# Kernel tuning notes

Hardware: AMD Instinct MI355X
Metric: run time of the kernel (lower is better)

The kernel has to match this reference:

```python
import jax, jax.numpy as jnp
import numpy as np

COMMITMENT_COST = 0.25


def setup_inputs() -> dict:
    key = jax.random.key(0)
    k1, k2 = jax.random.split(key)
    z_e = jax.random.normal(k1, (32, 256, 32, 32), dtype=jnp.float32)
    codebook = jax.random.normal(k2, (1024, 256), dtype=jnp.float32)
    return {"z_e": z_e, "codebook": codebook}


def reference(z_e, codebook):
    B, D, H, W = z_e.shape
    # (B, D, H, W) -> (N, D), N = B*H*W
    z_flat = jnp.transpose(z_e, (0, 2, 3, 1)).reshape(-1, D)
    # squared L2 distances to every codebook entry: (N, K)
    distances = (
        jnp.sum(z_flat * z_flat, axis=1, keepdims=True)
        - 2.0 * (z_flat @ codebook.T)
        + jnp.sum(codebook * codebook, axis=1)
    )
    codes = jnp.argmin(distances, axis=1)          # (N,)
    z_q = jnp.transpose(codebook[codes].reshape(B, H, W, D), (0, 3, 1, 2))
    # straight-through estimator
    z_q_st = z_e + jax.lax.stop_gradient(z_q - z_e)
    codebook_loss = jnp.mean((jax.lax.stop_gradient(z_q) - z_e) ** 2)
    commitment_loss = jnp.mean((z_q - jax.lax.stop_gradient(z_e)) ** 2)
    vq_loss = codebook_loss + COMMITMENT_COST * commitment_loss
    indices = codes.reshape(B, H, W)
    return z_q_st, indices, vq_loss
```

## Files before the change

### kernel.cpp

```cpp
#include <hip/hip_runtime.h>
#include <cstdint>
#include <cstddef>


typedef __attribute__((ext_vector_type(8))) short bf16x8;
typedef __attribute__((ext_vector_type(4))) float f32x4;

#define GL2LDS(g, l) __builtin_amdgcn_global_load_lds( \
    (__attribute__((address_space(1))) const void*)(g), \
    (__attribute__((address_space(3))) void*)(l), 16, 0, 0)

__device__ __forceinline__ unsigned short rne_bf16(float f) {
    unsigned u = __float_as_uint(f);
    return (unsigned short)((u + 0x7FFFu + ((u >> 16) & 1u)) >> 16);
}
__device__ __forceinline__ float bf16_to_f(unsigned short h) {
    return __uint_as_float((unsigned)h << 16);
}

__global__ __launch_bounds__(256)
void vq_cnorm_kernel(const float* __restrict__ cb, float* __restrict__ cnorm)
{
    const int k = blockIdx.x * 256 + threadIdx.x;
    const float4* row = reinterpret_cast<const float4*>(cb + (size_t)k * 256);
    float s0 = 0.f, s1 = 0.f, s2 = 0.f, s3 = 0.f;
#pragma unroll 8
    for (int i = 0; i < 64; ++i) {
        float4 v = row[i];
        s0 = fmaf(v.x, v.x, s0);
        s1 = fmaf(v.y, v.y, s1);
        s2 = fmaf(v.z, v.z, s2);
        s3 = fmaf(v.w, v.w, s3);
    }
    cnorm[k] = (s0 + s1) + (s2 + s3);
}

__global__ __launch_bounds__(256)
void vq_csplit_kernel(const float* __restrict__ cb, unsigned short* __restrict__ c0,
                      unsigned short* __restrict__ c1, unsigned short* __restrict__ c2,
                      unsigned long long* __restrict__ packed, float* __restrict__ loss)
{
    const int b = blockIdx.x, t = threadIdx.x;
    const int idx = b * 256 + t;
    if (t < 128) packed[b * 128 + t] = 0xFFFFFFFFFFFFFFFFull;
    if (b == 0 && t == 255) *loss = 0.f;

    float4 v = reinterpret_cast<const float4*>(cb)[idx];
    float f[4] = { v.x, v.y, v.z, v.w };
    ushort4 h0, h1, h2;
    unsigned short* p0[4] = { &h0.x, &h0.y, &h0.z, &h0.w };
    unsigned short* p1[4] = { &h1.x, &h1.y, &h1.z, &h1.w };
    unsigned short* p2[4] = { &h2.x, &h2.y, &h2.z, &h2.w };
#pragma unroll
    for (int j = 0; j < 4; ++j) {
        unsigned short b0 = rne_bf16(f[j]); float r1 = f[j] - bf16_to_f(b0);
        unsigned short b1 = rne_bf16(r1);   float r2 = r1 - bf16_to_f(b1);
        unsigned short b2 = rne_bf16(r2);
        *p0[j] = b0; *p1[j] = b1; *p2[j] = b2;
    }
    reinterpret_cast<ushort4*>(c0)[idx] = h0;
    reinterpret_cast<ushort4*>(c1)[idx] = h1;
    reinterpret_cast<ushort4*>(c2)[idx] = h2;
}

__global__ __launch_bounds__(256)
void vq_zsplit_kernel(const float* __restrict__ z, unsigned short* __restrict__ z0,
                      unsigned short* __restrict__ z1, unsigned short* __restrict__ z2)
{
    __shared__ float zl[64 * 264];
    const int t = threadIdx.x, blk = blockIdx.x;
    const int b = blk >> 4, hw0 = (blk & 15) << 6;
    const float* zb = z + ((size_t)b << 18) + hw0;
#pragma unroll 8
    for (int i = 0; i < 64; ++i) {
        int idx = i * 256 + t;
        int d = idx >> 6, hwl = idx & 63;
        zl[hwl * 264 + d] = zb[(size_t)d * 1024 + hwl];
    }
    __syncthreads();
    const int n0 = (b << 10) + hw0;
#pragma unroll
    for (int p = 0; p < 8; ++p) {
        const int hwl = p * 8 + (t >> 5);
        const int d0 = (t & 31) * 8;
        const float* src = &zl[hwl * 264 + d0];
        unsigned short h0[8], h1[8], h2[8];
#pragma unroll
        for (int j = 0; j < 8; ++j) {
            float f = src[j];
            unsigned short b0 = rne_bf16(f);  float r1 = f - bf16_to_f(b0);
            unsigned short b1 = rne_bf16(r1); float r2 = r1 - bf16_to_f(b1);
            unsigned short b2 = rne_bf16(r2);
            h0[j] = b0; h1[j] = b1; h2[j] = b2;
        }
        const size_t o = (size_t)(n0 + hwl) * 256 + d0;
        ushort4 a;
        a = ushort4{h0[0],h0[1],h0[2],h0[3]}; *reinterpret_cast<ushort4*>(z0 + o)     = a;
        a = ushort4{h0[4],h0[5],h0[6],h0[7]}; *reinterpret_cast<ushort4*>(z0 + o + 4) = a;
        a = ushort4{h1[0],h1[1],h1[2],h1[3]}; *reinterpret_cast<ushort4*>(z1 + o)     = a;
        a = ushort4{h1[4],h1[5],h1[6],h1[7]}; *reinterpret_cast<ushort4*>(z1 + o + 4) = a;
        a = ushort4{h2[0],h2[1],h2[2],h2[3]}; *reinterpret_cast<ushort4*>(z2 + o)     = a;
        a = ushort4{h2[4],h2[5],h2[6],h2[7]}; *reinterpret_cast<ushort4*>(z2 + o + 4) = a;
    }
}

__global__ __launch_bounds__(512, 2)
void vq_mfma_argmin_kernel(const unsigned short* __restrict__ zp,
                           const unsigned short* __restrict__ cp,
                           const float* __restrict__ cnorm,
                           unsigned long long* __restrict__ packed)
{
    __shared__ unsigned short Ld[2][2][2][256 * 32];

    const int tid = threadIdx.x, l = tid & 63, w = tid >> 6;
    const int wr = w >> 2, wc = w & 3;
    const int nid = ((blockIdx.x & 7) << 6) | (blockIdx.x >> 3);
    const int bm = nid >> 2, bn = nid & 3;
    const int arow = bm * 256, brow = bn * 256;

    f32x4 acc[8][4];
#pragma unroll
    for (int m = 0; m < 8; ++m)
#pragma unroll
        for (int n = 0; n < 4; ++n) acc[m][n] = f32x4{0.f, 0.f, 0.f, 0.f};

    const int srow  = l >> 2;
    const int selem = (((l & 3) ^ ((l >> 3) & 3))) << 3;

    const int lo16 = l & 15, hi4 = l >> 4;
    const int fco = ((hi4 ^ ((lo16 >> 1) & 3))) << 3;

#define STAGE(tt, mat, kk) do {                                               \
    const int seg_ = (tt) >> 2;                                               \
    const unsigned short* S_ = (mat)                                          \
        ? cp + (size_t)((0x211000 >> (seg_ << 2)) & 3) * 262144u              \
        : zp + (size_t)((0x010210 >> (seg_ << 2)) & 3) * 8388608u;            \
    const int R_  = (mat) ? brow : arow;                                      \
    const int KO_ = (((tt) & 3) << 6) + ((kk) << 5) + selem;                  \
    GL2LDS(S_ + (size_t)(R_ + (w * 2 + 0) * 16 + srow) * 256 + KO_,           \
           &Ld[(tt) & 1][mat][kk][(w * 2 + 0) * 512]);                        \
    GL2LDS(S_ + (size_t)(R_ + (w * 2 + 1) * 16 + srow) * 256 + KO_,           \
           &Ld[(tt) & 1][mat][kk][(w * 2 + 1) * 512]);                        \
} while (0)

#define VM4  asm volatile("s_waitcnt vmcnt(4)"  ::: "memory")
#define VM0  asm volatile("s_waitcnt vmcnt(0)"  ::: "memory")
#define NOPS ((void)0)
#define FNCE do { asm volatile("" ::: "memory");                              \
                  __builtin_amdgcn_sched_barrier(0); } while (0)
#define SBAR do { asm volatile("" ::: "memory");                              \
                  __builtin_amdgcn_s_barrier();                               \
                  __builtin_amdgcn_sched_barrier(0); } while (0)

#define PH(t, mh, kk, STAGESTMT, VMSTMT, BARSTMT) do {                        \
    const unsigned short* Ap_ = &Ld[(t) & 1][0][kk][0];                       \
    const unsigned short* Bp_ = &Ld[(t) & 1][1][kk][0];                       \
    bf16x8 a0, a1, a2, a3, b0, b1, b2, b3;                                    \
    a0 = *(const bf16x8*)&Ap_[(wr*128 + ((mh)*4+0)*16 + lo16)*32 + fco];      \
    a1 = *(const bf16x8*)&Ap_[(wr*128 + ((mh)*4+1)*16 + lo16)*32 + fco];      \
    a2 = *(const bf16x8*)&Ap_[(wr*128 + ((mh)*4+2)*16 + lo16)*32 + fco];      \
    a3 = *(const bf16x8*)&Ap_[(wr*128 + ((mh)*4+3)*16 + lo16)*32 + fco];      \
    b0 = *(const bf16x8*)&Bp_[(wc*64 + 0*16 + lo16)*32 + fco];                \
    b1 = *(const bf16x8*)&Bp_[(wc*64 + 1*16 + lo16)*32 + fco];                \
    b2 = *(const bf16x8*)&Bp_[(wc*64 + 2*16 + lo16)*32 + fco];                \
    b3 = *(const bf16x8*)&Bp_[(wc*64 + 3*16 + lo16)*32 + fco];                \
    STAGESTMT;                                                                \
    FNCE;                                                                     \
    __builtin_amdgcn_s_setprio(1);                                            \
    acc[(mh)*4+0][0] = __builtin_amdgcn_mfma_f32_16x16x32_bf16(a0, b0, acc[(mh)*4+0][0], 0,0,0); \
    acc[(mh)*4+0][1] = __builtin_amdgcn_mfma_f32_16x16x32_bf16(a0, b1, acc[(mh)*4+0][1], 0,0,0); \
    acc[(mh)*4+0][2] = __builtin_amdgcn_mfma_f32_16x16x32_bf16(a0, b2, acc[(mh)*4+0][2], 0,0,0); \
    acc[(mh)*4+0][3] = __builtin_amdgcn_mfma_f32_16x16x32_bf16(a0, b3, acc[(mh)*4+0][3], 0,0,0); \
    acc[(mh)*4+1][0] = __builtin_amdgcn_mfma_f32_16x16x32_bf16(a1, b0, acc[(mh)*4+1][0], 0,0,0); \
    acc[(mh)*4+1][1] = __builtin_amdgcn_mfma_f32_16x16x32_bf16(a1, b1, acc[(mh)*4+1][1], 0,0,0); \
    acc[(mh)*4+1][2] = __builtin_amdgcn_mfma_f32_16x16x32_bf16(a1, b2, acc[(mh)*4+1][2], 0,0,0); \
    acc[(mh)*4+1][3] = __builtin_amdgcn_mfma_f32_16x16x32_bf16(a1, b3, acc[(mh)*4+1][3], 0,0,0); \
    acc[(mh)*4+2][0] = __builtin_amdgcn_mfma_f32_16x16x32_bf16(a2, b0, acc[(mh)*4+2][0], 0,0,0); \
    acc[(mh)*4+2][1] = __builtin_amdgcn_mfma_f32_16x16x32_bf16(a2, b1, acc[(mh)*4+2][1], 0,0,0); \
    acc[(mh)*4+2][2] = __builtin_amdgcn_mfma_f32_16x16x32_bf16(a2, b2, acc[(mh)*4+2][2], 0,0,0); \
    acc[(mh)*4+2][3] = __builtin_amdgcn_mfma_f32_16x16x32_bf16(a2, b3, acc[(mh)*4+2][3], 0,0,0); \
    acc[(mh)*4+3][0] = __builtin_amdgcn_mfma_f32_16x16x32_bf16(a3, b0, acc[(mh)*4+3][0], 0,0,0); \
    acc[(mh)*4+3][1] = __builtin_amdgcn_mfma_f32_16x16x32_bf16(a3, b1, acc[(mh)*4+3][1], 0,0,0); \
    acc[(mh)*4+3][2] = __builtin_amdgcn_mfma_f32_16x16x32_bf16(a3, b2, acc[(mh)*4+3][2], 0,0,0); \
    acc[(mh)*4+3][3] = __builtin_amdgcn_mfma_f32_16x16x32_bf16(a3, b3, acc[(mh)*4+3][3], 0,0,0); \
    __builtin_amdgcn_s_setprio(0);                                            \
    VMSTMT;                                                                   \
    BARSTMT;                                                                  \
} while (0)

#define TILE(t, SA0, SB0, SA1, SB1, V2, V4)                                   \
    PH(t, 0, 0, SA0, NOPS, FNCE);                                             \
    PH(t, 1, 0, SB0, V2,   SBAR);                                             \
    PH(t, 0, 1, SA1, NOPS, FNCE);                                             \
    PH(t, 1, 1, SB1, V4,   SBAR)

    STAGE(0, 0, 0); STAGE(0, 1, 0); STAGE(0, 0, 1); STAGE(0, 1, 1);
    VM4;
    SBAR;

#pragma unroll 2
    for (int t = 0; t <= 22; ++t) {
        TILE(t, STAGE(t + 1, 0, 0), STAGE(t + 1, 1, 0),
                STAGE(t + 1, 0, 1), STAGE(t + 1, 1, 1), VM4, VM4);
    }
    TILE(23, NOPS, NOPS, NOPS, NOPS, VM0, NOPS);

#undef TILE
#undef PH
#undef STAGE

    int coln[4]; float cnv[4];
#pragma unroll
    for (int n = 0; n < 4; ++n) {
        coln[n] = brow + wc * 64 + n * 16 + lo16;
        cnv[n] = cnorm[coln[n]];
    }
#pragma unroll
    for (int m = 0; m < 8; ++m) {
#pragma unroll
        for (int j = 0; j < 4; ++j) {
            unsigned long long best = 0xFFFFFFFFFFFFFFFFull;
#pragma unroll
            for (int n = 0; n < 4; ++n) {
                float d = fmaf(-2.0f, acc[m][n][j], cnv[n]);
                unsigned u = __float_as_uint(d);
                u = (u & 0x80000000u) ? ~u : (u | 0x80000000u);
                unsigned long long pk = ((unsigned long long)u << 32) | (unsigned)coln[n];
                best = pk < best ? pk : best;
            }
#pragma unroll
            for (int mask = 1; mask <= 8; mask <<= 1) {
                unsigned long long o = __shfl_xor(best, mask, 64);
                best = o < best ? o : best;
            }
            if (lo16 == 0) {
                const int row = arow + wr * 128 + m * 16 + hi4 * 4 + j;
                atomicMin(&packed[row], best);
            }
        }
    }
}

__global__ __launch_bounds__(256, 2)
void vq_gather_packed_kernel(const float* __restrict__ cb, const float* __restrict__ z,
                             const unsigned long long* __restrict__ packed,
                             float* __restrict__ out_zq, float* __restrict__ out_idx,
                             float* __restrict__ loss)
{
    __shared__ float rows[64 * 257];
    __shared__ int   ks[64];
    __shared__ float wsum[4];

    const int t   = threadIdx.x;
    const int blk = blockIdx.x;
    const int b   = blk >> 4;
    const int hw0 = (blk & 15) << 6;
    const int n0  = blk << 6;

    if (t < 64) {
        const int k = (int)(packed[n0 + t] & 0xFFFFFFFFull);
        ks[t] = k;
        out_idx[n0 + t] = (float)k;
    }
    __syncthreads();

#pragma unroll 4
    for (int i = 0; i < 64; ++i) {
        rows[i * 257 + t] = cb[(size_t)ks[i] * 256 + t];
    }
    __syncthreads();

    const int dq = t >> 6;
    const int hw = t & 63;
    const size_t obase = ((size_t)b << 18) + hw0 + hw;
    float sum = 0.f;
#pragma unroll 4
    for (int dd = 0; dd < 64; ++dd) {
        const int d = (dq << 6) + dd;
        const float  q  = rows[hw * 257 + d];
        const size_t a  = obase + (size_t)d * 1024;
        const float  zv = z[a];
        out_zq[a] = q;
        const float diff = q - zv;
        sum = fmaf(diff, diff, sum);
    }
#pragma unroll
    for (int m = 1; m <= 32; m <<= 1) sum += __shfl_xor(sum, m, 64);
    if ((t & 63) == 0) wsum[t >> 6] = sum;
    __syncthreads();
    if (t == 0) {
        const float s = (wsum[0] + wsum[1]) + (wsum[2] + wsum[3]);
        atomicAdd(loss, s * (1.25f / 8388608.0f));
    }
}

__global__ __launch_bounds__(256)
void vq_transpose_kernel(const float* __restrict__ cb, float* __restrict__ ctT)
{
    __shared__ float tile[64 * 65];
    const int t  = threadIdx.x;
    const int kb = blockIdx.x >> 2, db = blockIdx.x & 3;
    const int k0 = kb << 6, d0 = db << 6;
#pragma unroll
    for (int i = 0; i < 16; ++i) {
        int idx = i * 256 + t;
        int r = idx >> 6, c = idx & 63;
        tile[r * 65 + c] = cb[(size_t)(k0 + r) * 256 + d0 + c];
    }
    __syncthreads();
#pragma unroll
    for (int i = 0; i < 16; ++i) {
        int idx = i * 256 + t;
        int r = idx >> 6, c = idx & 63;
        ctT[(size_t)(d0 + r) * 1024 + k0 + c] = tile[c * 65 + r];
    }
}

__global__ __launch_bounds__(256)
void vq_cnorm_fb_kernel(const float* __restrict__ cb, float* __restrict__ cnorm)
{
    const int k = blockIdx.x * 256 + threadIdx.x;
    const float4* row = reinterpret_cast<const float4*>(cb + (size_t)k * 256);
    float s0 = 0.f, s1 = 0.f, s2 = 0.f, s3 = 0.f;
#pragma unroll 8
    for (int i = 0; i < 64; ++i) {
        float4 v = row[i];
        s0 = fmaf(v.x, v.x, s0);
        s1 = fmaf(v.y, v.y, s1);
        s2 = fmaf(v.z, v.z, s2);
        s3 = fmaf(v.w, v.w, s3);
    }
    cnorm[k] = (s0 + s1) + (s2 + s3);
}

__global__ __launch_bounds__(512, 2)
void vq_argmin_kernel(const float* __restrict__ z, const float* __restrict__ ctT,
                      const float* __restrict__ cnorm, int* __restrict__ codes,
                      float* __restrict__ out_idx)
{
    __shared__ float zt[256 * 64];
    __shared__ float ct[16 * 256];
    const int t = threadIdx.x, tx = t & 63, ty = t >> 6, p0 = ty << 3;
    const int blk = blockIdx.x, b = blk >> 4, hw0 = (blk & 15) << 6;
    const float* zbase = z + ((size_t)b << 18) + hw0;
#pragma unroll
    for (int i = 0; i < 8; ++i) {
        int idx = i * 512 + t;
        int d = idx >> 4, c4 = (idx & 15) << 2;
        float4 v = *reinterpret_cast<const float4*>(zbase + (size_t)d * 1024 + c4);
        *reinterpret_cast<float4*>(&zt[d * 64 + c4]) = v;
    }
    float minv[8]; int mini[8];
#pragma unroll
    for (int i = 0; i < 8; ++i) { minv[i] = 3.0e38f; mini[i] = 0; }
    const float* zrd = &zt[p0];
    const float* crd = &ct[tx << 2];
    for (int kt = 0; kt < 4; ++kt) {
        const int k0 = kt << 8;
        float acc[8][4];
#pragma unroll
        for (int i = 0; i < 8; ++i)
#pragma unroll
            for (int j = 0; j < 4; ++j) acc[i][j] = 0.f;
        for (int dc = 0; dc < 16; ++dc) {
            const int d0 = dc << 4;
            __syncthreads();
#pragma unroll
            for (int i = 0; i < 2; ++i) {
                int idx = i * 512 + t;
                int r = idx >> 6, c4 = (idx & 63) << 2;
                float4 v = *reinterpret_cast<const float4*>(ctT + (size_t)(d0 + r) * 1024 + k0 + c4);
                *reinterpret_cast<float4*>(&ct[r * 256 + c4]) = v;
            }
            __syncthreads();
            const float* zp = zrd + d0 * 64;
#pragma unroll
            for (int d = 0; d < 16; ++d) {
                float4 za = *reinterpret_cast<const float4*>(zp + d * 64);
                float4 zb = *reinterpret_cast<const float4*>(zp + d * 64 + 4);
                float4 cc = *reinterpret_cast<const float4*>(crd + d * 256);
#define VQ_FMA_ROW(ii, zv)                          \
                acc[ii][0] = fmaf(zv, cc.x, acc[ii][0]); \
                acc[ii][1] = fmaf(zv, cc.y, acc[ii][1]); \
                acc[ii][2] = fmaf(zv, cc.z, acc[ii][2]); \
                acc[ii][3] = fmaf(zv, cc.w, acc[ii][3]);
                VQ_FMA_ROW(0, za.x) VQ_FMA_ROW(1, za.y) VQ_FMA_ROW(2, za.z) VQ_FMA_ROW(3, za.w)
                VQ_FMA_ROW(4, zb.x) VQ_FMA_ROW(5, zb.y) VQ_FMA_ROW(6, zb.z) VQ_FMA_ROW(7, zb.w)
#undef VQ_FMA_ROW
            }
        }
#pragma unroll
        for (int j = 0; j < 4; ++j) {
            const int k = k0 + (tx << 2) + j;
            const float cn = cnorm[k];
#pragma unroll
            for (int i = 0; i < 8; ++i) {
                float dist = fmaf(-2.0f, acc[i][j], cn);
                if (dist < minv[i]) { minv[i] = dist; mini[i] = k; }
            }
        }
    }
#pragma unroll
    for (int m = 1; m <= 32; m <<= 1) {
#pragma unroll
        for (int i = 0; i < 8; ++i) {
            float ov = __shfl_xor(minv[i], m, 64);
            int   oi = __shfl_xor(mini[i], m, 64);
            if (ov < minv[i] || (ov == minv[i] && oi < mini[i])) { minv[i] = ov; mini[i] = oi; }
        }
    }
    if (tx == 0) {
        const int n0 = (blk << 6) + p0;
#pragma unroll
        for (int i = 0; i < 8; ++i) {
            codes[n0 + i]   = mini[i];
            out_idx[n0 + i] = (float)mini[i];
        }
    }
}

__global__ __launch_bounds__(256, 2)
void vq_gather_kernel(const float* __restrict__ cb, const float* __restrict__ z,
                      const int* __restrict__ codes, float* __restrict__ out_zq,
                      float* __restrict__ loss)
{
    __shared__ float rows[64 * 257];
    __shared__ int   ks[64];
    __shared__ float wsum[4];
    const int t = threadIdx.x, blk = blockIdx.x;
    const int b = blk >> 4, hw0 = (blk & 15) << 6, n0 = blk << 6;
    if (t < 64) ks[t] = codes[n0 + t];
    __syncthreads();
#pragma unroll 4
    for (int i = 0; i < 64; ++i) rows[i * 257 + t] = cb[(size_t)ks[i] * 256 + t];
    __syncthreads();
    const int dq = t >> 6, hw = t & 63;
    const size_t obase = ((size_t)b << 18) + hw0 + hw;
    float sum = 0.f;
#pragma unroll 4
    for (int dd = 0; dd < 64; ++dd) {
        const int d = (dq << 6) + dd;
        const float  q  = rows[hw * 257 + d];
        const size_t a  = obase + (size_t)d * 1024;
        const float  zv = z[a];
        out_zq[a] = q;
        const float diff = q - zv;
        sum = fmaf(diff, diff, sum);
    }
#pragma unroll
    for (int m = 1; m <= 32; m <<= 1) sum += __shfl_xor(sum, m, 64);
    if ((t & 63) == 0) wsum[t >> 6] = sum;
    __syncthreads();
    if (t == 0) {
        const float s = (wsum[0] + wsum[1]) + (wsum[2] + wsum[3]);
        atomicAdd(loss, s * (1.25f / 8388608.0f));
    }
}

extern "C" void kernel_launch(void* const* d_in, const int* in_sizes, int n_in,
                              void* d_out, int out_size, void* d_ws, size_t ws_size,
                              hipStream_t stream)
{
    (void)in_sizes; (void)n_in; (void)out_size;

    const float* z  = (const float*)d_in[0];
    const float* cb = (const float*)d_in[1];

    float* out      = (float*)d_out;
    float* out_zq   = out;
    float* out_idx  = out + 8388608;
    float* out_loss = out + 8421376;

    const size_t NEED = 262144ull + 3ull * 16777216ull + 3ull * 524288ull + 4096ull;

    if (ws_size >= NEED) {
        unsigned long long* packed = (unsigned long long*)d_ws;
        unsigned short* z0 = (unsigned short*)((char*)d_ws + 262144);
        unsigned short* z1 = z0 + 8388608u;
        unsigned short* z2 = z1 + 8388608u;
        unsigned short* c0 = z2 + 8388608u;
        unsigned short* c1 = c0 + 262144u;
        unsigned short* c2 = c1 + 262144u;
        float* cnorm = (float*)(c2 + 262144u);

        vq_csplit_kernel<<<256, 256, 0, stream>>>(cb, c0, c1, c2, packed, out_loss);
        vq_cnorm_kernel<<<4, 256, 0, stream>>>(cb, cnorm);
        vq_zsplit_kernel<<<512, 256, 0, stream>>>(z, z0, z1, z2);
        vq_mfma_argmin_kernel<<<512, 512, 0, stream>>>(z0, c0, cnorm, packed);
        vq_gather_packed_kernel<<<512, 256, 0, stream>>>(cb, z, packed, out_zq, out_idx, out_loss);
    } else {
        float* ctT   = (float*)d_ws;
        float* cnorm = ctT + 256 * 1024;
        int*   codes = (int*)(cnorm + 1024);

        hipMemsetAsync(out_loss, 0, sizeof(float), stream);
        vq_transpose_kernel<<<64, 256, 0, stream>>>(cb, ctT);
        vq_cnorm_fb_kernel<<<4, 256, 0, stream>>>(cb, cnorm);
        vq_argmin_kernel<<<512, 512, 0, stream>>>(z, ctT, cnorm, codes, out_idx);
        vq_gather_kernel<<<512, 256, 0, stream>>>(cb, z, codes, out_zq, out_loss);
    }
}
```

Measured before the change: 172.2 us.

## Retile argmin GEMM to 256x128 blocks with triple-buffered LDS pipeline

Shrinks each block's tile from 256x256 to 256x128 codes, doubling the grid to 1024 blocks and halving per-wave accumulators. Staging moves from a double buffer to a three-stage LDS ring, issuing six async global-to-LDS loads two tiles ahead with one barrier per K-step. The aim is deeper latency hiding and better load balance across CUs. In exchange the z operand is reloaded twice as often, the launch bound drops to one block per CU, and LDS per block grows to 144KB.

New measurement: 180.1 us. 4.6% more time.

```diff
diff --git a/kernel.cpp b/kernel.cpp
--- a/kernel.cpp
+++ b/kernel.cpp
@@ -104,23 +104,23 @@
     }
 }
 
-__global__ __launch_bounds__(512, 2)
+__global__ __launch_bounds__(512, 1)
 void vq_mfma_argmin_kernel(const unsigned short* __restrict__ zp,
                            const unsigned short* __restrict__ cp,
                            const float* __restrict__ cnorm,
                            unsigned long long* __restrict__ packed)
 {
-    __shared__ unsigned short Ld[2][2][2][256 * 32];
+    __shared__ unsigned short Ld[3 * 24576];
 
     const int tid = threadIdx.x, l = tid & 63, w = tid >> 6;
-    const int wr = w >> 2, wc = w & 3;
-    const int nid = ((blockIdx.x & 7) << 6) | (blockIdx.x >> 3);
-    const int bm = nid >> 2, bn = nid & 3;
-    const int arow = bm * 256, brow = bn * 256;
-
-    f32x4 acc[8][4];
-#pragma unroll
-    for (int m = 0; m < 8; ++m)
+    const int wr = w >> 1, wc = w & 1;
+    const int nid = ((blockIdx.x & 7) << 7) | (blockIdx.x >> 3);
+    const int bm = nid >> 3, bn = nid & 7;
+    const int arow = bm * 256, brow = bn * 128;
+
+    f32x4 acc[4][4];
+#pragma unroll
+    for (int m = 0; m < 4; ++m)
 #pragma unroll
         for (int n = 0; n < 4; ++n) acc[m][n] = f32x4{0.f, 0.f, 0.f, 0.f};
 
@@ -130,20 +130,20 @@
     const int lo16 = l & 15, hi4 = l >> 4;
     const int fco = ((hi4 ^ ((lo16 >> 1) & 3))) << 3;
 
-#define STAGE(tt, mat, kk) do {                                               \
+#define STAGE6(tt, BUFP) do {                                                 \
     const int seg_ = (tt) >> 2;                                               \
-    const unsigned short* S_ = (mat)                                          \
-        ? cp + (size_t)((0x211000 >> (seg_ << 2)) & 3) * 262144u              \
-        : zp + (size_t)((0x010210 >> (seg_ << 2)) & 3) * 8388608u;            \
-    const int R_  = (mat) ? brow : arow;                                      \
-    const int KO_ = (((tt) & 3) << 6) + ((kk) << 5) + selem;                  \
-    GL2LDS(S_ + (size_t)(R_ + (w * 2 + 0) * 16 + srow) * 256 + KO_,           \
-           &Ld[(tt) & 1][mat][kk][(w * 2 + 0) * 512]);                        \
-    GL2LDS(S_ + (size_t)(R_ + (w * 2 + 1) * 16 + srow) * 256 + KO_,           \
-           &Ld[(tt) & 1][mat][kk][(w * 2 + 1) * 512]);                        \
+    const unsigned short* As_ = zp + (size_t)((0x010210 >> (seg_ << 2)) & 3) * 8388608u; \
+    const unsigned short* Bs_ = cp + (size_t)((0x211000 >> (seg_ << 2)) & 3) * 262144u;  \
+    const int KO_ = (((tt) & 3) << 6) + selem;                                \
+    GL2LDS(As_ + (size_t)(arow + w * 32 +  0 + srow) * 256 + KO_,      (BUFP) + (w * 32     ) * 32); \
+    GL2LDS(As_ + (size_t)(arow + w * 32 + 16 + srow) * 256 + KO_,      (BUFP) + (w * 32 + 16) * 32); \
+    GL2LDS(As_ + (size_t)(arow + w * 32 +  0 + srow) * 256 + KO_ + 32, (BUFP) + 8192 + (w * 32     ) * 32); \
+    GL2LDS(As_ + (size_t)(arow + w * 32 + 16 + srow) * 256 + KO_ + 32, (BUFP) + 8192 + (w * 32 + 16) * 32); \
+    GL2LDS(Bs_ + (size_t)(brow + w * 16 + srow) * 256 + KO_,           (BUFP) + 16384 + (w * 16) * 32); \
+    GL2LDS(Bs_ + (size_t)(brow + w * 16 + srow) * 256 + KO_ + 32,      (BUFP) + 16384 + 4096 + (w * 16) * 32); \
 } while (0)
 
-#define VM4  asm volatile("s_waitcnt vmcnt(4)"  ::: "memory")
+#define VM6  asm volatile("s_waitcnt vmcnt(6)"  ::: "memory")
 #define VM0  asm volatile("s_waitcnt vmcnt(0)"  ::: "memory")
 #define NOPS ((void)0)
 #define FNCE do { asm volatile("" ::: "memory");                              \
@@ -152,14 +152,32 @@
                   __builtin_amdgcn_s_barrier();                               \
                   __builtin_amdgcn_sched_barrier(0); } while (0)
 
-#define PH(t, mh, kk, STAGESTMT, VMSTMT, BARSTMT) do {                        \
-    const unsigned short* Ap_ = &Ld[(t) & 1][0][kk][0];                       \
-    const unsigned short* Bp_ = &Ld[(t) & 1][1][kk][0];                       \
+#define MFMA16(A0, A1, A2, A3, B0, B1, B2, B3)                                \
+    acc[0][0] = __builtin_amdgcn_mfma_f32_16x16x32_bf16(A0, B0, acc[0][0], 0,0,0); \
+    acc[0][1] = __builtin_amdgcn_mfma_f32_16x16x32_bf16(A0, B1, acc[0][1], 0,0,0); \
+    acc[0][2] = __builtin_amdgcn_mfma_f32_16x16x32_bf16(A0, B2, acc[0][2], 0,0,0); \
+    acc[0][3] = __builtin_amdgcn_mfma_f32_16x16x32_bf16(A0, B3, acc[0][3], 0,0,0); \
+    acc[1][0] = __builtin_amdgcn_mfma_f32_16x16x32_bf16(A1, B0, acc[1][0], 0,0,0); \
+    acc[1][1] = __builtin_amdgcn_mfma_f32_16x16x32_bf16(A1, B1, acc[1][1], 0,0,0); \
+    acc[1][2] = __builtin_amdgcn_mfma_f32_16x16x32_bf16(A1, B2, acc[1][2], 0,0,0); \
+    acc[1][3] = __builtin_amdgcn_mfma_f32_16x16x32_bf16(A1, B3, acc[1][3], 0,0,0); \
+    acc[2][0] = __builtin_amdgcn_mfma_f32_16x16x32_bf16(A2, B0, acc[2][0], 0,0,0); \
+    acc[2][1] = __builtin_amdgcn_mfma_f32_16x16x32_bf16(A2, B1, acc[2][1], 0,0,0); \
+    acc[2][2] = __builtin_amdgcn_mfma_f32_16x16x32_bf16(A2, B2, acc[2][2], 0,0,0); \
+    acc[2][3] = __builtin_amdgcn_mfma_f32_16x16x32_bf16(A2, B3, acc[2][3], 0,0,0); \
+    acc[3][0] = __builtin_amdgcn_mfma_f32_16x16x32_bf16(A3, B0, acc[3][0], 0,0,0); \
+    acc[3][1] = __builtin_amdgcn_mfma_f32_16x16x32_bf16(A3, B1, acc[3][1], 0,0,0); \
+    acc[3][2] = __builtin_amdgcn_mfma_f32_16x16x32_bf16(A3, B2, acc[3][2], 0,0,0); \
+    acc[3][3] = __builtin_amdgcn_mfma_f32_16x16x32_bf16(A3, B3, acc[3][3], 0,0,0)
+
+#define PH_T(BUFP, STAGESTMT, VMSTMT, BARSTMT) do {                           \
+    const unsigned short* Ap_ = (BUFP);                                       \
+    const unsigned short* Bp_ = (BUFP) + 16384;                               \
     bf16x8 a0, a1, a2, a3, b0, b1, b2, b3;                                    \
-    a0 = *(const bf16x8*)&Ap_[(wr*128 + ((mh)*4+0)*16 + lo16)*32 + fco];      \
-    a1 = *(const bf16x8*)&Ap_[(wr*128 + ((mh)*4+1)*16 + lo16)*32 + fco];      \
-    a2 = *(const bf16x8*)&Ap_[(wr*128 + ((mh)*4+2)*16 + lo16)*32 + fco];      \
-    a3 = *(const bf16x8*)&Ap_[(wr*128 + ((mh)*4+3)*16 + lo16)*32 + fco];      \
+    a0 = *(const bf16x8*)&Ap_[(wr*64 + 0*16 + lo16)*32 + fco];                \
+    a1 = *(const bf16x8*)&Ap_[(wr*64 + 1*16 + lo16)*32 + fco];                \
+    a2 = *(const bf16x8*)&Ap_[(wr*64 + 2*16 + lo16)*32 + fco];                \
+    a3 = *(const bf16x8*)&Ap_[(wr*64 + 3*16 + lo16)*32 + fco];                \
     b0 = *(const bf16x8*)&Bp_[(wc*64 + 0*16 + lo16)*32 + fco];                \
     b1 = *(const bf16x8*)&Bp_[(wc*64 + 1*16 + lo16)*32 + fco];                \
     b2 = *(const bf16x8*)&Bp_[(wc*64 + 2*16 + lo16)*32 + fco];                \
@@ -167,47 +185,41 @@
     STAGESTMT;                                                                \
     FNCE;                                                                     \
     __builtin_amdgcn_s_setprio(1);                                            \
-    acc[(mh)*4+0][0] = __builtin_amdgcn_mfma_f32_16x16x32_bf16(a0, b0, acc[(mh)*4+0][0], 0,0,0); \
-    acc[(mh)*4+0][1] = __builtin_amdgcn_mfma_f32_16x16x32_bf16(a0, b1, acc[(mh)*4+0][1], 0,0,0); \
-    acc[(mh)*4+0][2] = __builtin_amdgcn_mfma_f32_16x16x32_bf16(a0, b2, acc[(mh)*4+0][2], 0,0,0); \
-    acc[(mh)*4+0][3] = __builtin_amdgcn_mfma_f32_16x16x32_bf16(a0, b3, acc[(mh)*4+0][3], 0,0,0); \
-    acc[(mh)*4+1][0] = __builtin_amdgcn_mfma_f32_16x16x32_bf16(a1, b0, acc[(mh)*4+1][0], 0,0,0); \
-    acc[(mh)*4+1][1] = __builtin_amdgcn_mfma_f32_16x16x32_bf16(a1, b1, acc[(mh)*4+1][1], 0,0,0); \
-    acc[(mh)*4+1][2] = __builtin_amdgcn_mfma_f32_16x16x32_bf16(a1, b2, acc[(mh)*4+1][2], 0,0,0); \
-    acc[(mh)*4+1][3] = __builtin_amdgcn_mfma_f32_16x16x32_bf16(a1, b3, acc[(mh)*4+1][3], 0,0,0); \
-    acc[(mh)*4+2][0] = __builtin_amdgcn_mfma_f32_16x16x32_bf16(a2, b0, acc[(mh)*4+2][0], 0,0,0); \
-    acc[(mh)*4+2][1] = __builtin_amdgcn_mfma_f32_16x16x32_bf16(a2, b1, acc[(mh)*4+2][1], 0,0,0); \
-    acc[(mh)*4+2][2] = __builtin_amdgcn_mfma_f32_16x16x32_bf16(a2, b2, acc[(mh)*4+2][2], 0,0,0); \
-    acc[(mh)*4+2][3] = __builtin_amdgcn_mfma_f32_16x16x32_bf16(a2, b3, acc[(mh)*4+2][3], 0,0,0); \
-    acc[(mh)*4+3][0] = __builtin_amdgcn_mfma_f32_16x16x32_bf16(a3, b0, acc[(mh)*4+3][0], 0,0,0); \
-    acc[(mh)*4+3][1] = __builtin_amdgcn_mfma_f32_16x16x32_bf16(a3, b1, acc[(mh)*4+3][1], 0,0,0); \
-    acc[(mh)*4+3][2] = __builtin_amdgcn_mfma_f32_16x16x32_bf16(a3, b2, acc[(mh)*4+3][2], 0,0,0); \
-    acc[(mh)*4+3][3] = __builtin_amdgcn_mfma_f32_16x16x32_bf16(a3, b3, acc[(mh)*4+3][3], 0,0,0); \
+    MFMA16(a0, a1, a2, a3, b0, b1, b2, b3);                                   \
+    __builtin_amdgcn_s_setprio(0);                                            \
+    a0 = *(const bf16x8*)&Ap_[8192 + (wr*64 + 0*16 + lo16)*32 + fco];         \
+    a1 = *(const bf16x8*)&Ap_[8192 + (wr*64 + 1*16 + lo16)*32 + fco];         \
+    a2 = *(const bf16x8*)&Ap_[8192 + (wr*64 + 2*16 + lo16)*32 + fco];         \
+    a3 = *(const bf16x8*)&Ap_[8192 + (wr*64 + 3*16 + lo16)*32 + fco];         \
+    b0 = *(const bf16x8*)&Bp_[4096 + (wc*64 + 0*16 + lo16)*32 + fco];         \
+    b1 = *(const bf16x8*)&Bp_[4096 + (wc*64 + 1*16 + lo16)*32 + fco];         \
+    b2 = *(const bf16x8*)&Bp_[4096 + (wc*64 + 2*16 + lo16)*32 + fco];         \
+    b3 = *(const bf16x8*)&Bp_[4096 + (wc*64 + 3*16 + lo16)*32 + fco];         \
+    FNCE;                                                                     \
+    __builtin_amdgcn_s_setprio(1);                                            \
+    MFMA16(a0, a1, a2, a3, b0, b1, b2, b3);                                   \
     __builtin_amdgcn_s_setprio(0);                                            \
     VMSTMT;                                                                   \
     BARSTMT;                                                                  \
 } while (0)
 
-#define TILE(t, SA0, SB0, SA1, SB1, V2, V4)                                   \
-    PH(t, 0, 0, SA0, NOPS, FNCE);                                             \
-    PH(t, 1, 0, SB0, V2,   SBAR);                                             \
-    PH(t, 0, 1, SA1, NOPS, FNCE);                                             \
-    PH(t, 1, 1, SB1, V4,   SBAR)
-
-    STAGE(0, 0, 0); STAGE(0, 1, 0); STAGE(0, 0, 1); STAGE(0, 1, 1);
-    VM4;
+    STAGE6(0, Ld);
+    STAGE6(1, Ld + 24576);
+    VM6;
     SBAR;
 
-#pragma unroll 2
-    for (int t = 0; t <= 22; ++t) {
-        TILE(t, STAGE(t + 1, 0, 0), STAGE(t + 1, 1, 0),
-                STAGE(t + 1, 0, 1), STAGE(t + 1, 1, 1), VM4, VM4);
-    }
-    TILE(23, NOPS, NOPS, NOPS, NOPS, VM0, NOPS);
-
-#undef TILE
-#undef PH
-#undef STAGE
+    for (int t = 0; t < 21; t += 3) {
+        PH_T(Ld,             STAGE6(t + 2, Ld + 2 * 24576), VM6, SBAR);
+        PH_T(Ld + 24576,     STAGE6(t + 3, Ld),             VM6, SBAR);
+        PH_T(Ld + 2 * 24576, STAGE6(t + 4, Ld + 24576),     VM6, SBAR);
+    }
+    PH_T(Ld,             STAGE6(23, Ld + 2 * 24576), VM6, SBAR);
+    PH_T(Ld + 24576,     NOPS,                       VM0, SBAR);
+    PH_T(Ld + 2 * 24576, NOPS,                       NOPS, NOPS);
+
+#undef PH_T
+#undef MFMA16
+#undef STAGE6
 
     int coln[4]; float cnv[4];
 #pragma unroll
@@ -216,7 +228,7 @@
         cnv[n] = cnorm[coln[n]];
     }
 #pragma unroll
-    for (int m = 0; m < 8; ++m) {
+    for (int m = 0; m < 4; ++m) {
 #pragma unroll
         for (int j = 0; j < 4; ++j) {
             unsigned long long best = 0xFFFFFFFFFFFFFFFFull;
@@ -234,7 +246,7 @@
                 best = o < best ? o : best;
             }
             if (lo16 == 0) {
-                const int row = arow + wr * 128 + m * 16 + hi4 * 4 + j;
+                const int row = arow + wr * 64 + m * 16 + hi4 * 4 + j;
                 atomicMin(&packed[row], best);
             }
         }
@@ -486,7 +498,7 @@
         vq_csplit_kernel<<<256, 256, 0, stream>>>(cb, c0, c1, c2, packed, out_loss);
         vq_cnorm_kernel<<<4, 256, 0, stream>>>(cb, cnorm);
         vq_zsplit_kernel<<<512, 256, 0, stream>>>(z, z0, z1, z2);
-        vq_mfma_argmin_kernel<<<512, 512, 0, stream>>>(z0, c0, cnorm, packed);
+        vq_mfma_argmin_kernel<<<1024, 512, 0, stream>>>(z0, c0, cnorm, packed);
         vq_gather_packed_kernel<<<512, 256, 0, stream>>>(cb, z, packed, out_zq, out_idx, out_loss);
     } else {
         float* ctT   = (float*)d_ws;
```
